# Kernel optimization log

Measured on AMD Instinct MI355X. Metric: run time of the kernel, lower is better.

## Reference

```python
import jax, jax.numpy as jnp
import numpy as np

D_MODEL = 512
NUM_HEADS = 8
HEAD_DIM = D_MODEL // NUM_HEADS


def setup_inputs() -> dict:
    key = jax.random.key(0)
    ks = jax.random.split(key, 9)
    B, N, D = 2, 4096, D_MODEL
    scale = 1.0 / np.sqrt(D)
    inp = {
        "x": jax.random.normal(ks[0], (B, N, D), dtype=jnp.float32),
        "wq": jax.random.normal(ks[1], (D, D), dtype=jnp.float32) * scale,
        "bq": jnp.zeros((D,), dtype=jnp.float32),
        "wk": jax.random.normal(ks[2], (D, D), dtype=jnp.float32) * scale,
        "bk": jnp.zeros((D,), dtype=jnp.float32),
        "wv": jax.random.normal(ks[3], (D, D), dtype=jnp.float32) * scale,
        "bv": jnp.zeros((D,), dtype=jnp.float32),
        "wo": jax.random.normal(ks[4], (D, D), dtype=jnp.float32) * scale,
        "bo": jnp.zeros((D,), dtype=jnp.float32),
    }
    return inp


def reference(x, wq, bq, wk, bk, wv, bv, wo, bo):
    B, N, D = x.shape
    h, dh = NUM_HEADS, HEAD_DIM
    # QKV projections (torch Linear: x @ W.T + b); reshape to [B, h, N, dh]
    def proj(w, b):
        y = jnp.einsum('bnd,ed->bne', x, w) + b
        return y.reshape(B, N, h, dh).transpose(0, 2, 1, 3)
    q = proj(wq, bq)
    k = proj(wk, bk)
    v = proj(wv, bv)
    # scaled dot-product attention, full [B, h, N, N] scores (matches module)
    attn = jnp.einsum('bhqd,bhkd->bhqk', q, k) / jnp.sqrt(jnp.float32(dh)).astype(x.dtype)
    attn = jax.nn.softmax(attn, axis=-1)
    y = jnp.einsum('bhqk,bhkd->bhqd', attn, v)
    y = y.transpose(0, 2, 1, 3).reshape(B, N, D)
    # output projection
    return jnp.einsum('bnd,ed->bne', y, wo) + bo
```

## Files before the change

### kernel.cpp

```cpp
#include <hip/hip_runtime.h>
#include <hip/hip_bf16.h>

#define NN 4096
#define DD 512
#define HH 8
#define DH 64
#define BN 8192
#define PAIRS 16

typedef unsigned int uint32;
typedef __attribute__((ext_vector_type(8))) short short8;
typedef __attribute__((ext_vector_type(4))) float f32x4;

__device__ __forceinline__ unsigned short f2b(float x) {
    union { float f; uint32 u; } c; c.f = x;
    return (unsigned short)((c.u + 0x8000u) >> 16);
}
__device__ __forceinline__ uint32 pack2(float lo, float hi) {
    return (uint32)f2b(lo) | ((uint32)f2b(hi) << 16);
}
__device__ __forceinline__ uint32 cvtpk(float lo, float hi) {
    uint32 r;
    asm("v_cvt_pk_bf16_f32 %0, %1, %2" : "=v"(r) : "v"(lo), "v"(hi));
    return r;
}
__device__ __forceinline__ float expsc(float s) {
    return __builtin_amdgcn_exp2f(s);
}
#define QSCALE 0.18033688011112042f

__device__ __forceinline__ void gload16(const void* g, void* l) {
    __builtin_amdgcn_global_load_lds(
        (const __attribute__((address_space(1))) void*)g,
        (__attribute__((address_space(3))) void*)l, 16, 0, 0);
}

__global__ void detect_dtype(const uint32* __restrict__ xw, uint32* __restrict__ flag) {
    __shared__ int cnt;
    if (threadIdx.x == 0) cnt = 0;
    __syncthreads();
    int c = 0;
    for (int i = threadIdx.x; i < 1024; i += 64) {
        uint32 e = (xw[i] >> 7) & 0xFFu;
        if (e >= 110u && e <= 135u) c++;
    }
    atomicAdd(&cnt, c);
    __syncthreads();
    if (threadIdx.x == 0) *flag = (cnt < 512) ? 1u : 0u;
}

__global__ __launch_bounds__(256) void conv_x(const void* __restrict__ src,
                                              unsigned short* __restrict__ dst,
                                              const uint32* __restrict__ flagp) {
    int i0 = (blockIdx.x * 256 + threadIdx.x) * 8;
    if (*flagp) {
        const float4* s = (const float4*)src;
        float4 a = s[i0 >> 2], b = s[(i0 >> 2) + 1];
        uint4 o;
        o.x = pack2(a.x, a.y); o.y = pack2(a.z, a.w);
        o.z = pack2(b.x, b.y); o.w = pack2(b.z, b.w);
        *(uint4*)(dst + i0) = o;
    } else {
        *(uint4*)(dst + i0) = ((const uint4*)src)[i0 >> 3];
    }
}

__global__ __launch_bounds__(256) void conv_w(const void* s0, const void* s1,
                                              const void* s2, const void* s3,
                                              unsigned short* __restrict__ dst,
                                              const uint32* __restrict__ flagp) {
    int seg = blockIdx.x >> 7;
    const void* src = (seg == 0) ? s0 : (seg == 1) ? s1 : (seg == 2) ? s2 : s3;
    unsigned short* d = dst + (size_t)seg * DD * DD;
    int i0 = ((blockIdx.x & 127) * 256 + threadIdx.x) * 8;
    if (*flagp) {
        const float4* s = (const float4*)src;
        float4 a = s[i0 >> 2], b = s[(i0 >> 2) + 1];
        uint4 o;
        o.x = pack2(a.x, a.y); o.y = pack2(a.z, a.w);
        o.z = pack2(b.x, b.y); o.w = pack2(b.z, b.w);
        *(uint4*)(d + i0) = o;
    } else {
        *(uint4*)(d + i0) = ((const uint4*)src)[i0 >> 3];
    }
}

__global__ __launch_bounds__(256) void conv_b(const void* s0, const void* s1,
                                              const void* s2, const void* s3,
                                              float* __restrict__ dst,
                                              const uint32* __restrict__ flagp) {
    const void* sl[4] = { s0, s1, s2, s3 };
    int fp32mode = (int)*flagp;
    #pragma unroll
    for (int m = 0; m < 4; ++m) {
        #pragma unroll
        for (int j = 0; j < 2; ++j) {
            int i = threadIdx.x * 2 + j;
            float v;
            if (fp32mode) v = ((const float*)sl[m])[i];
            else {
                union { uint32 u; float f; } c;
                c.u = ((uint32)((const unsigned short*)sl[m])[i]) << 16;
                v = c.f;
            }
            dst[m * DD + i] = v;
        }
    }
}

__global__ __launch_bounds__(256) void qkv_gemm(
    const unsigned short* __restrict__ xb,
    const unsigned short* __restrict__ wsb,
    const float* __restrict__ bsf,
    unsigned short* __restrict__ Qb, unsigned short* __restrict__ Kb,
    unsigned short* __restrict__ VTg)
{
    __shared__ unsigned short As[128 * 32];
    __shared__ unsigned short Bs[128 * 32];
    const int tid = threadIdx.x;
    const int mat = blockIdx.x >> 8;
    const int rem = blockIdx.x & 255;
    const int nt = rem >> 6, mt = rem & 63;
    const int m0 = mt * 128, n0 = nt * 128;
    const int w = tid >> 6, lane = tid & 63, quad = lane >> 4, col = lane & 15;
    const int wr = w >> 1, wc = w & 1;
    const unsigned short* wm = wsb + (size_t)mat * DD * DD;
    const bool qk = (mat < 2);

    f32x4 acc[4][4];
    #pragma unroll
    for (int i = 0; i < 4; ++i)
        #pragma unroll
        for (int j = 0; j < 4; ++j)
            acc[i][j] = (f32x4){0.f, 0.f, 0.f, 0.f};

    for (int kt = 0; kt < 16; ++kt) {
        int k0 = kt * 32;
        __syncthreads();
        #pragma unroll
        for (int it = 0; it < 2; ++it) {
            int idx = tid + it * 256;
            int row = idx >> 2, c4 = idx & 3;
            unsigned short* lA = &As[(size_t)(it * 256 + w * 64) * 8];
            unsigned short* lB = &Bs[(size_t)(it * 256 + w * 64) * 8];
            gload16(xb + (size_t)(m0 + row) * DD + k0 + c4 * 8, lA);
            gload16(wm + (size_t)(n0 + row) * DD + k0 + c4 * 8, lB);
        }
        __syncthreads();
        if (qk) {
            short8 wf[4], xf[4];
            #pragma unroll
            for (int i = 0; i < 4; ++i)
                wf[i] = *(const short8*)&Bs[(wr * 64 + i * 16 + col) * 32 + quad * 8];
            #pragma unroll
            for (int j = 0; j < 4; ++j)
                xf[j] = *(const short8*)&As[(wc * 64 + j * 16 + col) * 32 + quad * 8];
            #pragma unroll
            for (int i = 0; i < 4; ++i)
                #pragma unroll
                for (int j = 0; j < 4; ++j)
                    acc[i][j] = __builtin_amdgcn_mfma_f32_16x16x32_bf16(
                        wf[i], xf[j], acc[i][j], 0, 0, 0);
        } else {
            short8 xf[4], wf[4];
            #pragma unroll
            for (int i = 0; i < 4; ++i)
                xf[i] = *(const short8*)&As[(wr * 64 + i * 16 + col) * 32 + quad * 8];
            #pragma unroll
            for (int j = 0; j < 4; ++j)
                wf[j] = *(const short8*)&Bs[(wc * 64 + j * 16 + col) * 32 + quad * 8];
            #pragma unroll
            for (int i = 0; i < 4; ++i)
                #pragma unroll
                for (int j = 0; j < 4; ++j)
                    acc[i][j] = __builtin_amdgcn_mfma_f32_16x16x32_bf16(
                        xf[i], wf[j], acc[i][j], 0, 0, 0);
        }
    }

    if (qk) {
        unsigned short* Om = (mat == 0) ? Qb : Kb;
        const float qs = (mat == 0) ? QSCALE : 1.0f;
        #pragma unroll
        for (int i = 0; i < 4; ++i) {
            int e0 = n0 + wr * 64 + i * 16 + quad * 4;
            float4 bj = *(const float4*)(bsf + mat * DD + e0);
            int h = e0 >> 6, jj0 = e0 & 63;
            #pragma unroll
            for (int j = 0; j < 4; ++j) {
                int g = m0 + wc * 64 + j * 16 + col;
                int b = g >> 12, n = g & (NN - 1);
                uint32 lo = pack2((acc[i][j][0] + bj.x) * qs, (acc[i][j][1] + bj.y) * qs);
                uint32 hi = pack2((acc[i][j][2] + bj.z) * qs, (acc[i][j][3] + bj.w) * qs);
                uint2 v; v.x = lo; v.y = hi;
                *(uint2*)(Om + ((size_t)((b << 3) + h) * NN + n) * DH + jj0) = v;
            }
        }
    } else {
        #pragma unroll
        for (int j = 0; j < 4; ++j) {
            int e = n0 + wc * 64 + j * 16 + col;
            float bj = bsf[2 * DD + e];
            int h = e >> 6, jj = e & 63;
            #pragma unroll
            for (int i = 0; i < 4; ++i) {
                int g0 = m0 + wr * 64 + i * 16 + quad * 4;
                int b = g0 >> 12, n = g0 & (NN - 1);
                uint32 lo = pack2(acc[i][j][0] + bj, acc[i][j][1] + bj);
                uint32 hi = pack2(acc[i][j][2] + bj, acc[i][j][3] + bj);
                uint2 v; v.x = lo; v.y = hi;
                *(uint2*)(VTg + ((size_t)((b << 3) + h) * DH + jj) * NN + n) = v;
            }
        }
    }
}

__global__ __launch_bounds__(512, 4) void attn_mfma(
    const unsigned short* __restrict__ Qb,
    const unsigned short* __restrict__ Kb,
    const unsigned short* __restrict__ VTg,
    unsigned short* __restrict__ Ob)
{
    __shared__ unsigned short Kt[2][64 * 72];
    __shared__ unsigned short Vt[2][64 * 72];

    const int tid  = threadIdx.x;
    const int w    = tid >> 6;
    const int lane = tid & 63;
    const int quad = lane >> 4;
    const int col  = lane & 15;
    const int pair = blockIdx.x >> 5;
    const int chunk = blockIdx.x & 31;
    const size_t base = (size_t)pair * NN;
    const int n0 = chunk * 128;
    const int qbase = w * 16;

    short8 qf[2];
    #pragma unroll
    for (int kk = 0; kk < 2; ++kk)
        qf[kk] = *(const short8*)(Qb +
            (base + n0 + qbase + col) * DH + kk * 32 + quad * 8);

    f32x4 accO[4];
    #pragma unroll
    for (int tc = 0; tc < 4; ++tc) accO[tc] = (f32x4){0.f, 0.f, 0.f, 0.f};
    float lsum = 0.f;

    const int skey = tid >> 3;
    const int sc8  = (tid & 7) * 8;
    const unsigned short* Kg = Kb + base * DH;
    const unsigned short* Vg = VTg + (size_t)pair * DH * NN;

    uint4 kreg = *(const uint4*)(Kg + (size_t)skey * DH + sc8);
    uint4 vreg = *(const uint4*)(Vg + (size_t)skey * NN + sc8);
    *(uint4*)&Kt[0][skey * 72 + sc8] = kreg;
    *(uint4*)&Vt[0][skey * 72 + sc8] = vreg;
    kreg = *(const uint4*)(Kg + (size_t)(64 + skey) * DH + sc8);
    vreg = *(const uint4*)(Vg + (size_t)skey * NN + 64 + sc8);
    __syncthreads();

    for (int kt = 0; kt < NN / 64; ++kt) {
        const int buf = kt & 1;
        if (kt + 1 < NN / 64) {
            *(uint4*)&Kt[buf ^ 1][skey * 72 + sc8] = kreg;
            *(uint4*)&Vt[buf ^ 1][skey * 72 + sc8] = vreg;
            int tn = (kt + 2 < NN / 64) ? kt + 2 : 0;
            kreg = *(const uint4*)(Kg + (size_t)(tn * 64 + skey) * DH + sc8);
            vreg = *(const uint4*)(Vg + (size_t)skey * NN + tn * 64 + sc8);
        }
        const unsigned short* Kc = &Kt[buf][0];
        const unsigned short* Vc = &Vt[buf][0];

        short8 pf[2];
        #pragma unroll
        for (int half = 0; half < 2; ++half) {
            f32x4 s0 = (f32x4){0.f, 0.f, 0.f, 0.f};
            f32x4 s1 = (f32x4){0.f, 0.f, 0.f, 0.f};
            __builtin_amdgcn_s_setprio(1);
            #pragma unroll
            for (int kk = 0; kk < 2; ++kk) {
                short8 kf0 = *(const short8*)&Kc[((half * 2 + 0) * 16 + col) * 72 + kk * 32 + quad * 8];
                short8 kf1 = *(const short8*)&Kc[((half * 2 + 1) * 16 + col) * 72 + kk * 32 + quad * 8];
                s0 = __builtin_amdgcn_mfma_f32_16x16x32_bf16(kf0, qf[kk], s0, 0, 0, 0);
                s1 = __builtin_amdgcn_mfma_f32_16x16x32_bf16(kf1, qf[kk], s1, 0, 0, 0);
            }
            __builtin_amdgcn_s_setprio(0);

            float p00 = expsc(s0[0]), p01 = expsc(s0[1]);
            float p02 = expsc(s0[2]), p03 = expsc(s0[3]);
            float p10 = expsc(s1[0]), p11 = expsc(s1[1]);
            float p12 = expsc(s1[2]), p13 = expsc(s1[3]);
            lsum += ((p00 + p01) + (p02 + p03)) + ((p10 + p11) + (p12 + p13));
            uint32 a0 = cvtpk(p00, p01);
            uint32 a1 = cvtpk(p02, p03);
            uint32 b0 = cvtpk(p10, p11);
            uint32 b1 = cvtpk(p12, p13);
            asm("v_permlane32_swap_b32 %0, %1" : "+v"(a0), "+v"(b0));
            asm("v_permlane32_swap_b32 %0, %1" : "+v"(a1), "+v"(b1));
            asm("v_permlane16_swap_b32 %0, %1" : "+v"(a0), "+v"(b0));
            asm("v_permlane16_swap_b32 %0, %1" : "+v"(a1), "+v"(b1));
            union { uint32 u[4]; short8 v; } pu;
            pu.u[0] = a0; pu.u[1] = a1; pu.u[2] = b0; pu.u[3] = b1;
            pf[half] = pu.v;
        }

        __builtin_amdgcn_s_setprio(1);
        #pragma unroll
        for (int tc = 0; tc < 4; ++tc) {
            short8 vf0 = *(const short8*)&Vc[(tc * 16 + col) * 72 + quad * 8];
            short8 vf1 = *(const short8*)&Vc[(tc * 16 + col) * 72 + 32 + quad * 8];
            accO[tc] = __builtin_amdgcn_mfma_f32_16x16x32_bf16(pf[0], vf0, accO[tc], 0, 0, 0);
            accO[tc] = __builtin_amdgcn_mfma_f32_16x16x32_bf16(pf[1], vf1, accO[tc], 0, 0, 0);
        }
        __builtin_amdgcn_s_setprio(0);

        __syncthreads();
    }

    lsum += __shfl_xor(lsum, 16);
    lsum += __shfl_xor(lsum, 32);

    float inv[4];
    #pragma unroll
    for (int r = 0; r < 4; ++r)
        inv[r] = 1.f / __shfl(lsum, quad * 4 + r);

    #pragma unroll
    for (int tc = 0; tc < 4; ++tc)
        #pragma unroll
        for (int r = 0; r < 4; ++r) {
            float v = accO[tc][r] * inv[r];
            Ob[(base + n0 + qbase + quad * 4 + r) * DH + tc * 16 + col] = f2b(v);
        }
}

__global__ __launch_bounds__(256) void out_gemm(
    const unsigned short* __restrict__ Ob,
    const unsigned short* __restrict__ wob,
    const float* __restrict__ bof,
    const uint32* __restrict__ flagp,
    void* __restrict__ outp)
{
    __shared__ unsigned short As[128 * 32];
    __shared__ unsigned short Bs[128 * 32];
    const int tid = threadIdx.x;
    const int nt = blockIdx.x >> 6, mt = blockIdx.x & 63;
    const int m0 = mt * 128, n0 = nt * 128;
    const int w = tid >> 6, lane = tid & 63, quad = lane >> 4, col = lane & 15;
    const int wr = w >> 1, wc = w & 1;
    const int fp32mode = (int)*flagp;

    f32x4 acc[4][4];
    #pragma unroll
    for (int i = 0; i < 4; ++i)
        #pragma unroll
        for (int j = 0; j < 4; ++j)
            acc[i][j] = (f32x4){0.f, 0.f, 0.f, 0.f};

    for (int kt = 0; kt < 16; ++kt) {
        int k0 = kt * 32;
        int h = k0 >> 6, koff = k0 & 63;
        __syncthreads();
        #pragma unroll
        for (int it = 0; it < 2; ++it) {
            int idx = tid + it * 256;
            int row = idx >> 2, c4 = idx & 3;
            int g = m0 + row, b = g >> 12, n = g & (NN - 1);
            unsigned short* lA = &As[(size_t)(it * 256 + w * 64) * 8];
            unsigned short* lB = &Bs[(size_t)(it * 256 + w * 64) * 8];
            gload16(Ob + ((size_t)((b << 3) + h) * NN + n) * DH + koff + c4 * 8, lA);
            gload16(wob + (size_t)(n0 + row) * DD + k0 + c4 * 8, lB);
        }
        __syncthreads();
        short8 wf[4], yf[4];
        #pragma unroll
        for (int i = 0; i < 4; ++i)
            wf[i] = *(const short8*)&Bs[(wr * 64 + i * 16 + col) * 32 + quad * 8];
        #pragma unroll
        for (int j = 0; j < 4; ++j)
            yf[j] = *(const short8*)&As[(wc * 64 + j * 16 + col) * 32 + quad * 8];
        #pragma unroll
        for (int i = 0; i < 4; ++i)
            #pragma unroll
            for (int j = 0; j < 4; ++j)
                acc[i][j] = __builtin_amdgcn_mfma_f32_16x16x32_bf16(
                    wf[i], yf[j], acc[i][j], 0, 0, 0);
    }

    #pragma unroll
    for (int i = 0; i < 4; ++i) {
        int e0 = n0 + wr * 64 + i * 16 + quad * 4;
        float4 bj = *(const float4*)(bof + e0);
        #pragma unroll
        for (int j = 0; j < 4; ++j) {
            int g = m0 + wc * 64 + j * 16 + col;
            float v0 = acc[i][j][0] + bj.x;
            float v1 = acc[i][j][1] + bj.y;
            float v2 = acc[i][j][2] + bj.z;
            float v3 = acc[i][j][3] + bj.w;
            if (fp32mode) {
                float4 o; o.x = v0; o.y = v1; o.z = v2; o.w = v3;
                *(float4*)((float*)outp + (size_t)g * DD + e0) = o;
            } else {
                uint2 o; o.x = pack2(v0, v1); o.y = pack2(v2, v3);
                *(uint2*)((unsigned short*)outp + (size_t)g * DD + e0) = o;
            }
        }
    }
}

extern "C" void kernel_launch(void* const* d_in, const int* in_sizes, int n_in,
                              void* d_out, int out_size, void* d_ws, size_t ws_size,
                              hipStream_t stream) {
    char* p = (char*)d_ws;
    uint32* flag = (uint32*)p;                  p += 256;
    unsigned short* xb  = (unsigned short*)p;   p += (size_t)BN * DD * 2;
    unsigned short* wsb = (unsigned short*)p;   p += (size_t)4 * DD * DD * 2;
    float*          bsf = (float*)p;            p += (size_t)4 * DD * 4;
    unsigned short* Qb  = (unsigned short*)p;   p += (size_t)PAIRS * NN * DH * 2;
    unsigned short* Kb  = (unsigned short*)p;   p += (size_t)PAIRS * NN * DH * 2;
    unsigned short* VTg = (unsigned short*)p;   p += (size_t)PAIRS * NN * DH * 2;
    unsigned short* Ob  = (unsigned short*)p;   p += (size_t)PAIRS * NN * DH * 2;

    detect_dtype<<<1, 64, 0, stream>>>((const uint32*)d_in[0], flag);
    conv_x<<<BN * DD / 2048, 256, 0, stream>>>(d_in[0], xb, flag);
    conv_w<<<512, 256, 0, stream>>>(d_in[1], d_in[3], d_in[5], d_in[7], wsb, flag);
    conv_b<<<1, 256, 0, stream>>>(d_in[2], d_in[4], d_in[6], d_in[8], bsf, flag);
    qkv_gemm<<<768, 256, 0, stream>>>(xb, wsb, bsf, Qb, Kb, VTg);
    attn_mfma<<<PAIRS * 32, 512, 0, stream>>>(Qb, Kb, VTg, Ob);
    out_gemm<<<256, 256, 0, stream>>>(Ob, wsb + (size_t)3 * DD * DD,
                                      bsf + 3 * DD, flag, d_out);
}
```

Before: 226.7 us.

## Split attention key range across two blocks and combine partials in new kernel

The attention kernel now splits each query chunk's key sequence into two halves handled by separate blocks, doubling the grid. Each block writes unnormalized fp32 output partials and row sums. A new combine kernel adds the two halves, normalizes, and writes the bf16 output that feeds the output projection. This is meant to raise occupancy and parallelism on a grid that did not fill the GPU. The cost is extra fp32 global memory traffic and an added kernel launch. The launch-bounds minimum blocks also rises from 4 to 8, which may squeeze the register budget.

```diff
diff --git a/kernel.cpp b/kernel.cpp
--- a/kernel.cpp
+++ b/kernel.cpp
@@ -12,6 +12,9 @@
 typedef __attribute__((ext_vector_type(8))) short short8;
 typedef __attribute__((ext_vector_type(4))) float f32x4;
 
+__device__ __forceinline__ float blo(uint32 u) {
+    union { uint32 i; float f; } c; c.i = u << 16; return c.f;
+}
 __device__ __forceinline__ unsigned short f2b(float x) {
     union { float f; uint32 u; } c; c.f = x;
     return (unsigned short)((c.u + 0x8000u) >> 16);
@@ -215,11 +218,12 @@
     }
 }
 
-__global__ __launch_bounds__(512, 4) void attn_mfma(
+__global__ __launch_bounds__(512, 8) void attn_mfma(
     const unsigned short* __restrict__ Qb,
     const unsigned short* __restrict__ Kb,
     const unsigned short* __restrict__ VTg,
-    unsigned short* __restrict__ Ob)
+    float* __restrict__ Op0, float* __restrict__ Op1,
+    float* __restrict__ lpart)
 {
     __shared__ unsigned short Kt[2][64 * 72];
     __shared__ unsigned short Vt[2][64 * 72];
@@ -229,11 +233,14 @@
     const int lane = tid & 63;
     const int quad = lane >> 4;
     const int col  = lane & 15;
-    const int pair = blockIdx.x >> 5;
+    const int pair  = blockIdx.x >> 6;
+    const int split = (blockIdx.x >> 5) & 1;
     const int chunk = blockIdx.x & 31;
     const size_t base = (size_t)pair * NN;
     const int n0 = chunk * 128;
     const int qbase = w * 16;
+    const int k0t = split * 32;
+    const int kend = k0t + 32;
 
     short8 qf[2];
     #pragma unroll
@@ -251,20 +258,20 @@
     const unsigned short* Kg = Kb + base * DH;
     const unsigned short* Vg = VTg + (size_t)pair * DH * NN;
 
-    uint4 kreg = *(const uint4*)(Kg + (size_t)skey * DH + sc8);
-    uint4 vreg = *(const uint4*)(Vg + (size_t)skey * NN + sc8);
+    uint4 kreg = *(const uint4*)(Kg + (size_t)(k0t * 64 + skey) * DH + sc8);
+    uint4 vreg = *(const uint4*)(Vg + (size_t)skey * NN + k0t * 64 + sc8);
     *(uint4*)&Kt[0][skey * 72 + sc8] = kreg;
     *(uint4*)&Vt[0][skey * 72 + sc8] = vreg;
-    kreg = *(const uint4*)(Kg + (size_t)(64 + skey) * DH + sc8);
-    vreg = *(const uint4*)(Vg + (size_t)skey * NN + 64 + sc8);
+    kreg = *(const uint4*)(Kg + (size_t)((k0t + 1) * 64 + skey) * DH + sc8);
+    vreg = *(const uint4*)(Vg + (size_t)skey * NN + (k0t + 1) * 64 + sc8);
     __syncthreads();
 
-    for (int kt = 0; kt < NN / 64; ++kt) {
+    for (int kt = k0t; kt < kend; ++kt) {
         const int buf = kt & 1;
-        if (kt + 1 < NN / 64) {
+        if (kt + 1 < kend) {
             *(uint4*)&Kt[buf ^ 1][skey * 72 + sc8] = kreg;
             *(uint4*)&Vt[buf ^ 1][skey * 72 + sc8] = vreg;
-            int tn = (kt + 2 < NN / 64) ? kt + 2 : 0;
+            int tn = (kt + 2 < kend) ? kt + 2 : k0t;
             kreg = *(const uint4*)(Kg + (size_t)(tn * 64 + skey) * DH + sc8);
             vreg = *(const uint4*)(Vg + (size_t)skey * NN + tn * 64 + sc8);
         }
@@ -320,18 +327,33 @@
     lsum += __shfl_xor(lsum, 16);
     lsum += __shfl_xor(lsum, 32);
 
-    float inv[4];
-    #pragma unroll
-    for (int r = 0; r < 4; ++r)
-        inv[r] = 1.f / __shfl(lsum, quad * 4 + r);
-
+    float* Op = split ? Op1 : Op0;
     #pragma unroll
     for (int tc = 0; tc < 4; ++tc)
         #pragma unroll
-        for (int r = 0; r < 4; ++r) {
-            float v = accO[tc][r] * inv[r];
-            Ob[(base + n0 + qbase + quad * 4 + r) * DH + tc * 16 + col] = f2b(v);
-        }
+        for (int r = 0; r < 4; ++r)
+            Op[(base + n0 + qbase + quad * 4 + r) * DH + tc * 16 + col] = accO[tc][r];
+    if (lane < 16)
+        lpart[(size_t)split * PAIRS * NN + base + n0 + qbase + lane] = lsum;
+}
+
+__global__ __launch_bounds__(256) void combine(
+    const float* __restrict__ Op0, const float* __restrict__ Op1,
+    const float* __restrict__ lpart, unsigned short* __restrict__ Ob)
+{
+    int g = blockIdx.x * 256 + threadIdx.x;
+    int row = g >> 3;
+    int d0 = (g & 7) * 8;
+    const float4* a = (const float4*)(Op0 + (size_t)row * DH + d0);
+    const float4* b = (const float4*)(Op1 + (size_t)row * DH + d0);
+    float4 a0 = a[0], a1 = a[1], b0 = b[0], b1 = b[1];
+    float inv = 1.f / (lpart[row] + lpart[(size_t)PAIRS * NN + row]);
+    uint4 o;
+    o.x = pack2((a0.x + b0.x) * inv, (a0.y + b0.y) * inv);
+    o.y = pack2((a0.z + b0.z) * inv, (a0.w + b0.w) * inv);
+    o.z = pack2((a1.x + b1.x) * inv, (a1.y + b1.y) * inv);
+    o.w = pack2((a1.z + b1.z) * inv, (a1.w + b1.w) * inv);
+    *(uint4*)(Ob + (size_t)row * DH + d0) = o;
 }
 
 __global__ __launch_bounds__(256) void out_gemm(
@@ -420,14 +442,18 @@
     unsigned short* Qb  = (unsigned short*)p;   p += (size_t)PAIRS * NN * DH * 2;
     unsigned short* Kb  = (unsigned short*)p;   p += (size_t)PAIRS * NN * DH * 2;
     unsigned short* VTg = (unsigned short*)p;   p += (size_t)PAIRS * NN * DH * 2;
-    unsigned short* Ob  = (unsigned short*)p;   p += (size_t)PAIRS * NN * DH * 2;
+    float*          Op0 = (float*)p;            p += (size_t)PAIRS * NN * DH * 4;
+    float*          Op1 = (float*)p;            p += (size_t)PAIRS * NN * DH * 4;
+    float*          lpart = (float*)p;          p += (size_t)2 * PAIRS * NN * 4;
+    unsigned short* Ob  = Qb;
 
     detect_dtype<<<1, 64, 0, stream>>>((const uint32*)d_in[0], flag);
     conv_x<<<BN * DD / 2048, 256, 0, stream>>>(d_in[0], xb, flag);
     conv_w<<<512, 256, 0, stream>>>(d_in[1], d_in[3], d_in[5], d_in[7], wsb, flag);
     conv_b<<<1, 256, 0, stream>>>(d_in[2], d_in[4], d_in[6], d_in[8], bsf, flag);
     qkv_gemm<<<768, 256, 0, stream>>>(xb, wsb, bsf, Qb, Kb, VTg);
-    attn_mfma<<<PAIRS * 32, 512, 0, stream>>>(Qb, Kb, VTg, Ob);
+    attn_mfma<<<PAIRS * 64, 512, 0, stream>>>(Qb, Kb, VTg, Op0, Op1, lpart);
+    combine<<<PAIRS * NN * DH / (8 * 256), 256, 0, stream>>>(Op0, Op1, lpart, Ob);
     out_gemm<<<256, 256, 0, stream>>>(Ob, wsb + (size_t)3 * DD * DD,
                                       bsf + 3 * DD, flag, d_out);
 }
```

Result: slower. 333.0 us (+46.9%).
